# Kernel tuning notes

Hardware: AMD Instinct MI355X
Metric: run time of the kernel (lower is better)

The kernel has to match this reference:

```python
import jax, jax.numpy as jnp
import numpy as np


def setup_inputs() -> dict:
    key = jax.random.key(0)
    d = jax.random.normal(key, (262144, 256), dtype=jnp.float32)
    return {"d": d}


def reference(d) -> jnp.ndarray:
    # torch: norm((d^T d) * I - I) * 0.001
    # (d^T d) * I keeps only the diagonal, i.e. per-column sum of squares.
    # Frobenius norm of diag(s) - I == sqrt(sum((s_j - 1)^2)).
    col_sq = jnp.sum(d * d, axis=0)            # [m] diagonal of d^T d
    loss = jnp.sqrt(jnp.sum((col_sq - 1.0) ** 2))
    return 0.001 * loss
```

## Files before the change

### kernel.cpp

```cpp
#include <hip/hip_runtime.h>
#include <math.h>


#define NROW   262144
#define NCOL   256
#define NCOLV  64
#define GRID   2048
#define ITERS  (NROW / 4 / GRID)

__global__ __launch_bounds__(256) void colsq_kernel(
        const float4* __restrict__ d, float* __restrict__ g_col) {
    const int tid   = threadIdx.x;
    const int c4    = tid & 63;
    const int r_off = tid >> 6;

    float4 acc = make_float4(0.f, 0.f, 0.f, 0.f);

    const size_t base_rg = (size_t)blockIdx.x * ITERS;
#pragma unroll 4
    for (int i = 0; i < ITERS; ++i) {
        const size_t row = (base_rg + i) * 4 + r_off;
        const float4 v = d[row * NCOLV + c4];
        acc.x += v.x * v.x;
        acc.y += v.y * v.y;
        acc.z += v.z * v.z;
        acc.w += v.w * v.w;
    }

    __shared__ float lds[4 * NCOL];
    float4* l4 = (float4*)lds;
    l4[r_off * NCOLV + c4] = acc;
    __syncthreads();
    float s = lds[tid] + lds[NCOL + tid] + lds[2 * NCOL + tid] + lds[3 * NCOL + tid];
    atomicAdd(&g_col[tid], s);
}

__global__ __launch_bounds__(256) void finalize_kernel(
        const float* __restrict__ g_col, float* __restrict__ out) {
    const int tid = threadIdx.x;
    float diff = g_col[tid] - 1.0f;
    float v = diff * diff;
#pragma unroll
    for (int off = 32; off > 0; off >>= 1)
        v += __shfl_down(v, off, 64);
    __shared__ float ws[4];
    if ((tid & 63) == 0) ws[tid >> 6] = v;
    __syncthreads();
    if (tid == 0) {
        float t = ws[0] + ws[1] + ws[2] + ws[3];
        out[0] = 0.001f * sqrtf(t);
    }
}

extern "C" void kernel_launch(void* const* d_in, const int* in_sizes, int n_in,
                              void* d_out, int out_size, void* d_ws, size_t ws_size,
                              hipStream_t stream) {
    const float4* d  = (const float4*)d_in[0];
    float* g_col     = (float*)d_ws;
    float* out       = (float*)d_out;

    hipMemsetAsync(g_col, 0, NCOL * sizeof(float), stream);
    colsq_kernel<<<GRID, 256, 0, stream>>>(d, g_col);
    finalize_kernel<<<1, 256, 0, stream>>>(g_col, out);
}
```

Baseline: 364.2 us.

## Fuse finalize into column-sum kernel via last-block counter, nontemporal loads

Drops the separate finalize launch. An atomic block counter lets the last block finishing the column sums compute the Frobenius loss in place. Loads now use nontemporal vector loads with a deeper unroll to stream the 256 MB input. This saves one kernel launch and a dependency gap, at the cost of a threadfence and an extra atomic in every block.

```diff
diff --git a/kernel.cpp b/kernel.cpp
--- a/kernel.cpp
+++ b/kernel.cpp
@@ -8,58 +8,64 @@
 #define GRID   2048
 #define ITERS  (NROW / 4 / GRID)
 
+typedef float v4f __attribute__((ext_vector_type(4)));
+
+
 __global__ __launch_bounds__(256) void colsq_kernel(
-        const float4* __restrict__ d, float* __restrict__ g_col) {
+        const v4f* __restrict__ d, float* __restrict__ g_col,
+        unsigned* __restrict__ cnt, float* __restrict__ out) {
     const int tid   = threadIdx.x;
     const int c4    = tid & 63;
     const int r_off = tid >> 6;
 
-    float4 acc = make_float4(0.f, 0.f, 0.f, 0.f);
+    v4f acc = (v4f)(0.f);
 
     const size_t base_rg = (size_t)blockIdx.x * ITERS;
-#pragma unroll 4
+#pragma unroll 8
     for (int i = 0; i < ITERS; ++i) {
         const size_t row = (base_rg + i) * 4 + r_off;
-        const float4 v = d[row * NCOLV + c4];
-        acc.x += v.x * v.x;
-        acc.y += v.y * v.y;
-        acc.z += v.z * v.z;
-        acc.w += v.w * v.w;
+        const v4f v = __builtin_nontemporal_load(&d[row * NCOLV + c4]);
+        acc += v * v;
     }
 
     __shared__ float lds[4 * NCOL];
-    float4* l4 = (float4*)lds;
+    v4f* l4 = (v4f*)lds;
     l4[r_off * NCOLV + c4] = acc;
     __syncthreads();
     float s = lds[tid] + lds[NCOL + tid] + lds[2 * NCOL + tid] + lds[3 * NCOL + tid];
     atomicAdd(&g_col[tid], s);
-}
 
-__global__ __launch_bounds__(256) void finalize_kernel(
-        const float* __restrict__ g_col, float* __restrict__ out) {
-    const int tid = threadIdx.x;
-    float diff = g_col[tid] - 1.0f;
-    float v = diff * diff;
+    __shared__ int is_last;
+    __threadfence();
+    if (tid == 0) {
+        unsigned old = atomicAdd(cnt, 1u);
+        is_last = (old == GRID - 1);
+    }
+    __syncthreads();
+    if (is_last) {
+        __threadfence();
+        float sj = atomicAdd(&g_col[tid], 0.0f);
+        float diff = sj - 1.0f;
+        float v = diff * diff;
 #pragma unroll
-    for (int off = 32; off > 0; off >>= 1)
-        v += __shfl_down(v, off, 64);
-    __shared__ float ws[4];
-    if ((tid & 63) == 0) ws[tid >> 6] = v;
-    __syncthreads();
-    if (tid == 0) {
-        float t = ws[0] + ws[1] + ws[2] + ws[3];
-        out[0] = 0.001f * sqrtf(t);
+        for (int off = 32; off > 0; off >>= 1)
+            v += __shfl_down(v, off, 64);
+        __shared__ float ws[4];
+        if ((tid & 63) == 0) ws[tid >> 6] = v;
+        __syncthreads();
+        if (tid == 0)
+            out[0] = 0.001f * sqrtf(ws[0] + ws[1] + ws[2] + ws[3]);
     }
 }
 
 extern "C" void kernel_launch(void* const* d_in, const int* in_sizes, int n_in,
                               void* d_out, int out_size, void* d_ws, size_t ws_size,
                               hipStream_t stream) {
-    const float4* d  = (const float4*)d_in[0];
+    const v4f* d     = (const v4f*)d_in[0];
     float* g_col     = (float*)d_ws;
+    unsigned* cnt    = (unsigned*)((char*)d_ws + NCOL * sizeof(float));
     float* out       = (float*)d_out;
 
-    hipMemsetAsync(g_col, 0, NCOL * sizeof(float), stream);
-    colsq_kernel<<<GRID, 256, 0, stream>>>(d, g_col);
-    finalize_kernel<<<1, 256, 0, stream>>>(g_col, out);
+    (void)hipMemsetAsync(d_ws, 0, 2048, stream);
+    colsq_kernel<<<GRID, 256, 0, stream>>>(d, g_col, cnt, out);
 }
```

After: 683.2 us. 1.88x slower.
